# Kernel optimization log

Hardware: AMD Instinct MI355X
Metric: run time of the kernel (lower is better)

The kernel has to match this reference:

```python
import jax, jax.numpy as jnp
import numpy as np

T, B, C = 4, 2, 128
LT, LH, LW = 8, 32, 32
NUM_HEADS = 8
HEAD_DIM = C // NUM_HEADS
THETA = 0.7
V_TH = 1.0
TAU = 2.0  # spikingjelly LIFNode default tau
N_WIN = (2, 2, 2)
TOPK = 4
EPS = 1e-5
ATAN_ALPHA = 2.0  # spikingjelly surrogate.ATan default


@jax.custom_vjp
def spike(x):
    return (x >= 0.0).astype(x.dtype)

def _spike_fwd(x):
    return spike(x), x

def _spike_bwd(x, g):
    s = (jnp.pi / 2.0) * ATAN_ALPHA * x
    return (g * (ATAN_ALPHA / 2.0) / (1.0 + s * s),)

spike.defvjp(_spike_fwd, _spike_bwd)


def lif(x_seq):
    """Multi-step LIF: v'=v+(x-v)/tau, spike at v>=V_TH, hard reset to 0 (detached)."""
    def step(v, x):
        v = v + (x - v) / TAU
        s = spike(v - V_TH)
        v = v * (1.0 - jax.lax.stop_gradient(s))  # detach_reset, v_reset=0
        return v, s
    _, s_seq = jax.lax.scan(step, jnp.zeros_like(x_seq[0]), x_seq)
    return s_seq


def bn(x, gamma, beta):
    # BatchNorm3d(track_running_stats=False) on [T*B, C, D, H, W]: batch stats per channel
    mean = x.mean(axis=(0, 1, 3, 4, 5), keepdims=True)
    var = x.var(axis=(0, 1, 3, 4, 5), keepdims=True)
    shp = (1, 1, -1, 1, 1, 1)
    return (x - mean) * jax.lax.rsqrt(var + EPS) * gamma.reshape(shp) + beta.reshape(shp)


def conv3d(x, w, pad):
    t, b = x.shape[:2]
    y = jax.lax.conv_general_dilated(
        x.reshape((t * b,) + x.shape[2:]), w,
        window_strides=(1, 1, 1), padding=[(pad, pad)] * 3,
        dimension_numbers=('NCDHW', 'OIDHW', 'NCDHW'))
    return y.reshape((t, b) + y.shape[1:])


def cdc_t(x, w):
    out = conv3d(x, w, 1)
    # central-difference temporal term: 1x1x1 conv with summed first/last temporal slices
    kd = w[:, :, 0].sum((-1, -2)) + w[:, :, 2].sum((-1, -2))  # [O, I]
    return out - THETA * jnp.einsum('oi,tbidhw->tbodhw', kd, x)


def to_wins(t):
    wt, wh, ww = N_WIN
    Tn, Bn, Cn, Lt, Lh, Lw = t.shape
    lt, lh, lw = Lt // wt, Lh // wh, Lw // ww
    t = t.reshape(Tn, Bn, Cn, wt, lt, wh, lh, ww, lw)
    t = t.transpose(0, 1, 3, 5, 7, 4, 6, 8, 2)
    return t.reshape(Tn, Bn, wt * wh * ww, lt * lh * lw, Cn)


def setup_inputs() -> dict:
    key = jax.random.key(0)
    ks = jax.random.split(key, 4)
    x = jax.random.normal(ks[0], (T, B, C, LT, LH, LW), jnp.float32)
    qw = jax.random.normal(ks[1], (C, C, 3, 3, 3), jnp.float32) / np.sqrt(C * 27)
    kw = jax.random.normal(ks[2], (C, C), jnp.float32) / np.sqrt(C)
    pw = jax.random.normal(ks[3], (C, C), jnp.float32) / np.sqrt(C)
    ones = jnp.ones((C,), jnp.float32)
    zeros = jnp.zeros((C,), jnp.float32)
    return {"x": x, "qw": qw, "q_gamma": ones, "q_beta": zeros,
            "kw": kw, "k_gamma": ones, "k_beta": zeros,
            "v_gamma": ones, "v_beta": zeros,
            "pw": pw, "p_gamma": ones, "p_beta": zeros}


def reference(x, qw, q_gamma, q_beta, kw, k_gamma, k_beta,
              v_gamma, v_beta, pw, p_gamma, p_beta):
    Tn, Bn, Cn, Lt, Lh, Lw = x.shape
    wt, wh, ww = N_WIN
    num_wins = wt * wh * ww
    lt, lh, lw = Lt // wt, Lh // wh, Lw // ww

    q_real = bn(cdc_t(x, qw), q_gamma, q_beta)
    k_real = bn(jnp.einsum('oi,tbidhw->tbodhw', kw, x), k_gamma, k_beta)

    # region-level routing from pre-spike activations
    q_region = to_wins(q_real).mean(axis=(0, 3))  # [B, W, C]
    k_region = to_wins(k_real).mean(axis=(0, 3))
    a_r = jnp.einsum('bwc,bvc->bwv', q_region, k_region) * (HEAD_DIM ** -0.5)
    k_eff = min(TOPK, num_wins)
    _, idx = jax.lax.top_k(a_r, k_eff)  # [B, W, k]

    q = lif(q_real)
    k = lif(k_real)
    v = lif(bn(x, v_gamma, v_beta))
    q_w = to_wins(q)  # [T,B,W,S,C]
    k_w = to_wins(k)
    v_w = to_wins(v)

    # gather routed windows per (batch, target window), mean-aggregate over top-k
    gather = jax.vmap(lambda src_b, idx_b: src_b[:, idx_b], in_axes=(1, 0), out_axes=1)
    k_agg = gather(k_w, idx).mean(axis=3)  # [T,B,W,S,C]
    v_agg = gather(v_w, idx).mean(axis=3)

    S = q_w.shape[3]
    q_h = q_w.reshape(Tn, Bn, num_wins, S, NUM_HEADS, HEAD_DIM)
    k_h = k_agg.reshape(Tn, Bn, num_wins, S, NUM_HEADS, HEAD_DIM)
    v_h = v_agg.reshape(Tn, Bn, num_wins, S, NUM_HEADS, HEAD_DIM)

    attn = (q_h * k_h).sum(axis=5, keepdims=True)  # [T,B,W,S,H,1]
    attn = lif(attn)
    out = (attn * v_h).reshape(Tn, Bn, num_wins, S, Cn)

    out = out.reshape(Tn, Bn, wt, wh, ww, lt, lh, lw, Cn)
    out = out.transpose(0, 1, 8, 2, 5, 3, 6, 4, 7).reshape(Tn, Bn, Cn, Lt, Lh, Lw)

    out = lif(out)
    out = bn(jnp.einsum('oi,tbidhw->tbodhw', pw, out), p_gamma, p_beta)
    return out
```

## Files before the change

kernel.cpp:

```cpp
#include <hip/hip_runtime.h>

#define TT 4
#define BB 2
#define CC 128
#define DD 8
#define HHH 32
#define WWW 32
#define PP (DD*HHH*WWW)
#define TSTRIDE (BB*CC*PP)
#define NWIN 8
#define SSS 1024
#define NHEAD 8
#define HDIM 16
#define THETA 0.7f
#define VTH 1.0f
#define NPERC (TT*BB*PP)
#define EPSf 1e-5f

typedef unsigned short ushortT;
typedef _Float16 half_t;
typedef _Float16 f16x8 __attribute__((ext_vector_type(8)));
typedef float    f32x16 __attribute__((ext_vector_type(16)));

typedef const __attribute__((address_space(1))) void* as1_cvp;
typedef __attribute__((address_space(3))) void* as3_vp;

__global__ __launch_bounds__(256) void prep_wmodT(const float* __restrict__ qw,
                                                  float* __restrict__ wmodT) {
    int oi = blockIdx.x*256 + threadIdx.x;
    if (oi >= CC*CC) return;
    int o  = oi >> 7;
    int ic = oi & 127;
    const float* wp = qw + (size_t)oi*27;
    float kd = 0.f;
    #pragma unroll
    for (int t=0; t<9; t++) kd += wp[t] + wp[18+t];
    #pragma unroll
    for (int t=0; t<27; t++) {
        float v = wp[t] - ((t==13) ? THETA*kd : 0.f);
        wmodT[((size_t)o*27 + t)*CC + ic] = v;
    }
}

__global__ __launch_bounds__(256) void prep_wfrag(const float* __restrict__ wmodT,
                                                  half_t* __restrict__ wfrag) {
    int id = blockIdx.x*256 + threadIdx.x;
    if (id >= 8*27*4*64) return;
    int lane = id & 63;
    int r = id >> 6;
    int m = r & 3; r >>= 2;
    int t = r % 27;
    int kb = r / 27;
    int o   = m*32 + (lane & 31);
    int ic0 = kb*16 + (lane>>5)*8;
    size_t base = ((size_t)(id>>6))*2*64*8 + (size_t)lane*8;
    #pragma unroll
    for (int j=0;j<8;j++){
        float v = wmodT[((size_t)o*27 + t)*CC + ic0 + j];
        half_t h = (half_t)v;
        half_t l = (half_t)(v - (float)h);
        wfrag[base + 0*64*8 + j] = h;
        wfrag[base + 1*64*8 + j] = l;
    }
}

__global__ __launch_bounds__(256) void prep_w1frag(const float* __restrict__ W,
                                                   half_t* __restrict__ frag) {
    int id = blockIdx.x*256 + threadIdx.x;
    if (id >= 2048) return;
    int lane = id & 63;
    int r = id >> 6;
    int m = r & 3;
    int kb = r >> 2;
    int o   = m*32 + (lane & 31);
    int ic0 = kb*16 + (lane>>5)*8;
    size_t base = ((size_t)(kb*4+m))*2*64*8 + (size_t)lane*8;
    #pragma unroll
    for (int j=0;j<8;j++){
        float v = W[(size_t)o*CC + ic0 + j];
        half_t h = (half_t)v;
        half_t l = (half_t)(v - (float)h);
        frag[base + 0*64*8 + j] = h;
        frag[base + 1*64*8 + j] = l;
    }
}

__global__ __launch_bounds__(256) void build_xsplit(const float* __restrict__ x,
                                                    half_t* __restrict__ xsp) {
    int id = blockIdx.x*256 + threadIdx.x;
    if (id >= 8*16*8*34*34) return;
    int wt = id % 34; int r = id/34;
    int hp = r % 34;  r /= 34;
    int dz = r % 8;   r /= 8;
    int icg = r & 15; int tb = r >> 4;
    bool inb = (hp>=1) & (hp<=32) & (wt>=1) & (wt<=32);
    half_t h8[8], l8[8];
    #pragma unroll
    for (int j=0;j<8;j++){
        float v = 0.f;
        if (inb)
            v = x[((size_t)(tb*CC + icg*8+j))*PP + (size_t)dz*1024 + (hp-1)*32 + (wt-1)];
        half_t h = (half_t)v;
        half_t l = (half_t)(v - (float)h);
        h8[j]=h; l8[j]=l;
    }
    #pragma unroll
    for (int sp=0; sp<2; sp++){
        size_t gu = (((((size_t)tb*2 + sp)*16 + icg)*8 + dz)*34 + hp)*34 + wt;
        half_t* dst = xsp + gu*8;
        const half_t* src = (sp==0)?h8:l8;
        #pragma unroll
        for (int j=0;j<8;j++) dst[j] = src[j];
    }
}

__global__ __launch_bounds__(256,2) void conv_mfma2(const half_t* __restrict__ xsp,
                                                    const half_t* __restrict__ wfrag,
                                                    float* __restrict__ y0,
                                                    float* __restrict__ y1) {
    __shared__ half_t slab[3264*8];
    int tid  = threadIdx.x;
    int wid  = tid >> 6;
    int lane = tid & 63;
    int ln   = lane & 31;
    int half_ = lane >> 5;
    int hg = blockIdx.x;
    int dp = blockIdx.y;
    int z  = blockIdx.z;
    int tb = z >> 1, kh = z & 1;
    int H0 = hg*4, d0 = dp*2;
    float* y = kh ? y1 : y0;

    f32x16 acc[2][4];
    #pragma unroll
    for (int dt=0;dt<2;dt++)
        #pragma unroll
        for (int m=0;m<4;m++)
            #pragma unroll
            for (int i=0;i<16;i++) acc[dt][m][i] = 0.f;

    f16x8 ca[4][2];
    #pragma unroll
    for (int m=0;m<4;m++)
        #pragma unroll
        for (int sp=0;sp<2;sp++)
            ca[m][sp] = *(const f16x8*)&wfrag[((((size_t)(kh*4*27)*4 + m)*2+sp)*64 + lane)*8];

    #pragma unroll 1
    for (int kk=0; kk<4; kk++) {
        int kb = kh*4 + kk;
        __syncthreads();
        #pragma unroll 1
        for (int u = tid; u < 3264; u += 256) {
            int sp  = u / 1632;
            int r   = u - sp*1632;
            int icg = r / 816;
            int p   = r - icg*816;
            int dz  = p / 204;
            int r3  = p - dz*204;
            int hp  = r3 / 34;
            int wt  = r3 - hp*34;
            int dd  = d0 - 1 + dz;
            half_t* ldst = &slab[(size_t)u*8];
            if ((unsigned)dd < 8u) {
                size_t gu = (((((size_t)tb*2 + sp)*16 + (kb*2+icg))*8 + dd)*34 + (H0+hp))*34 + wt;
                __builtin_amdgcn_global_load_lds((as1_cvp)&xsp[gu*8], (as3_vp)ldst, 16, 0, 0);
            } else {
                ulonglong2 zz; zz.x = 0; zz.y = 0;
                *(ulonglong2*)ldst = zz;
            }
        }
        __syncthreads();
        #pragma unroll 1
        for (int t=0; t<27; t++) {
            int dz=t/9; int rr=t-dz*9; int dh=rr/3; int dw=rr-dh*3;
            f16x8 cb[2][2];
            #pragma unroll
            for (int dt=0;dt<2;dt++){
                int bpos = (dt+dz)*204 + (wid+dh)*34 + ln + dw;
                #pragma unroll
                for (int sp=0;sp<2;sp++)
                    cb[dt][sp] = *(const f16x8*)&slab[(size_t)((sp*2+half_)*816 + bpos)*8];
            }
            f16x8 na[4][2];
            int nt  = (t<26)? t+1 : 0;
            int nkb = (t<26)? kb  : ((kk<3)? kb+1 : kb);
            #pragma unroll
            for (int m=0;m<4;m++)
                #pragma unroll
                for (int sp=0;sp<2;sp++)
                    na[m][sp] = *(const f16x8*)&wfrag[((((size_t)(nkb*27+nt)*4+m)*2+sp)*64 + lane)*8];
            #pragma unroll
            for (int dt=0;dt<2;dt++)
                #pragma unroll
                for (int m=0;m<4;m++) acc[dt][m] = __builtin_amdgcn_mfma_f32_32x32x16_f16(ca[m][0], cb[dt][0], acc[dt][m],0,0,0);
            #pragma unroll
            for (int dt=0;dt<2;dt++)
                #pragma unroll
                for (int m=0;m<4;m++) acc[dt][m] = __builtin_amdgcn_mfma_f32_32x32x16_f16(ca[m][0], cb[dt][1], acc[dt][m],0,0,0);
            #pragma unroll
            for (int dt=0;dt<2;dt++)
                #pragma unroll
                for (int m=0;m<4;m++) acc[dt][m] = __builtin_amdgcn_mfma_f32_32x32x16_f16(ca[m][1], cb[dt][0], acc[dt][m],0,0,0);
            #pragma unroll
            for (int m=0;m<4;m++)
                #pragma unroll
                for (int sp=0;sp<2;sp++) ca[m][sp] = na[m][sp];
        }
    }
    int h = H0 + wid;
    #pragma unroll
    for (int dt=0; dt<2; dt++) {
        #pragma unroll
        for (int m=0; m<4; m++) {
            #pragma unroll
            for (int reg=0; reg<16; reg++) {
                int row = (reg&3) + 8*(reg>>2) + 4*half_;
                int o = m*32 + row;
                y[((size_t)tb*CC + o)*PP + (d0+dt)*1024 + h*32 + ln] = acc[dt][m][reg];
            }
        }
    }
}

__global__ __launch_bounds__(256) void conv_add(float* __restrict__ q,
                                                const float* __restrict__ p1) {
    size_t i = ((size_t)blockIdx.x*256 + threadIdx.x)*4;
    float4 a = *(const float4*)&q[i];
    float4 b = *(const float4*)&p1[i];
    a.x+=b.x; a.y+=b.y; a.z+=b.z; a.w+=b.w;
    *(float4*)&q[i] = a;
}

__global__ __launch_bounds__(256) void kgemm_mfma(const half_t* __restrict__ xsp,
                                                  const half_t* __restrict__ wk,
                                                  float* __restrict__ y) {
    int tid  = threadIdx.x;
    int wid  = tid >> 6;
    int lane = tid & 63;
    int ln   = lane & 31;
    int half_ = lane >> 5;
    int hg = blockIdx.x, d = blockIdx.y, tb = blockIdx.z;
    int h = hg*4 + wid;

    f32x16 acc[4];
    #pragma unroll
    for (int m=0;m<4;m++)
        #pragma unroll
        for (int i=0;i<16;i++) acc[m][i] = 0.f;

    #pragma unroll 2
    for (int kb=0; kb<8; kb++) {
        f16x8 b[2];
        #pragma unroll
        for (int sp=0; sp<2; sp++) {
            size_t gu = (((((size_t)tb*2 + sp)*16 + (kb*2+half_))*8 + d)*34 + (h+1))*34 + (ln+1);
            b[sp] = *(const f16x8*)&xsp[gu*8];
        }
        #pragma unroll
        for (int m=0; m<4; m++) {
            const half_t* wb = wk + ((size_t)(kb*4+m))*2*64*8 + (size_t)lane*8;
            f16x8 a0 = *(const f16x8*)&wb[0*64*8];
            f16x8 a1 = *(const f16x8*)&wb[1*64*8];
            acc[m] = __builtin_amdgcn_mfma_f32_32x32x16_f16(a0, b[0], acc[m],0,0,0);
            acc[m] = __builtin_amdgcn_mfma_f32_32x32x16_f16(a0, b[1], acc[m],0,0,0);
            acc[m] = __builtin_amdgcn_mfma_f32_32x32x16_f16(a1, b[0], acc[m],0,0,0);
        }
    }
    #pragma unroll
    for (int m=0; m<4; m++) {
        #pragma unroll
        for (int reg=0; reg<16; reg++) {
            int row = (reg&3) + 8*(reg>>2) + 4*half_;
            int o = m*32 + row;
            y[((size_t)tb*CC + o)*PP + d*1024 + h*32 + ln] = acc[m][reg];
        }
    }
}

__global__ __launch_bounds__(256) void pgemm_mfma(const ushortT* __restrict__ spkb,
                                                  const half_t* __restrict__ wp,
                                                  float* __restrict__ y) {
    int tid  = threadIdx.x;
    int wid  = tid >> 6;
    int lane = tid & 63;
    int ln   = lane & 31;
    int half_ = lane >> 5;
    int hg = blockIdx.x, d = blockIdx.y, tb = blockIdx.z;
    int h = hg*4 + wid;
    int p = d*1024 + h*32 + ln;

    f32x16 acc[4];
    #pragma unroll
    for (int m=0;m<4;m++)
        #pragma unroll
        for (int i=0;i<16;i++) acc[m][i] = 0.f;

    #pragma unroll 2
    for (int kb=0; kb<8; kb++) {
        f16x8 b = *(const f16x8*)&spkb[(((size_t)tb*16 + (kb*2+half_))*PP + p)*8];
        #pragma unroll
        for (int m=0; m<4; m++) {
            const half_t* wb = wp + ((size_t)(kb*4+m))*2*64*8 + (size_t)lane*8;
            f16x8 a0 = *(const f16x8*)&wb[0*64*8];
            f16x8 a1 = *(const f16x8*)&wb[1*64*8];
            acc[m] = __builtin_amdgcn_mfma_f32_32x32x16_f16(a0, b, acc[m],0,0,0);
            acc[m] = __builtin_amdgcn_mfma_f32_32x32x16_f16(a1, b, acc[m],0,0,0);
        }
    }
    #pragma unroll
    for (int m=0; m<4; m++) {
        #pragma unroll
        for (int reg=0; reg<16; reg++) {
            int row = (reg&3) + 8*(reg>>2) + 4*half_;
            int o = m*32 + row;
            y[((size_t)tb*CC + o)*PP + p] = acc[m][reg];
        }
    }
}

__global__ __launch_bounds__(128) void win_stats(const float* __restrict__ q,
        const float* __restrict__ k, const float* __restrict__ x,
        float* __restrict__ rsum, float* __restrict__ rsq) {
    int blk = blockIdx.x;
    int src = blk >> 11;
    int r   = blk & 2047;
    const float* base = (src==0) ? q : ((src==1) ? k : x);
    int c  = r & 127;
    int wi = (r >> 7) & 7;
    int b  = r >> 10;
    int wd = wi>>2, wh = (wi>>1)&1, ww = wi&1;
    int tid = threadIdx.x;
    float s=0.f, s2=0.f;
    for (int t=0;t<TT;t++){
        const float* p = base + ((size_t)(t*BB+b)*CC + c)*PP;
        for (int si=tid; si<SSS; si+=128){
            int ld = si>>8, lh=(si>>4)&15, lw=si&15;
            float v = p[((wd*4+ld)<<10) + ((wh*16+lh)<<5) + (ww*16+lw)];
            s += v; s2 += v*v;
        }
    }
    __shared__ float ls[128], ls2[128];
    ls[tid]=s; ls2[tid]=s2; __syncthreads();
    for (int off=64;off>0;off>>=1){
        if(tid<off){ ls[tid]+=ls[tid+off]; ls2[tid]+=ls2[tid+off]; }
        __syncthreads();
    }
    if (tid==0){ rsum[blk]=ls[0]; rsq[blk]=ls2[0]; }
}

__global__ __launch_bounds__(384) void stats_fin(const float* __restrict__ rsum,
        const float* __restrict__ rsq, float* __restrict__ sums) {
    int tid = threadIdx.x;
    int src = tid >> 7, c = tid & 127;
    float s=0.f, s2=0.f;
    for (int bw=0; bw<16; bw++){
        int idx = src*2048 + bw*128 + c;
        s  += rsum[idx];
        s2 += rsq[idx];
    }
    sums[src*256 + c]       = s;
    sums[src*256 + 128 + c] = s2;
}

__global__ __launch_bounds__(128) void route_topk(const float* __restrict__ qreg,
        const float* __restrict__ kreg,
        const float* __restrict__ qsum, const float* __restrict__ qsq,
        const float* __restrict__ ksum, const float* __restrict__ ksq,
        const float* __restrict__ qg, const float* __restrict__ qb,
        const float* __restrict__ kg, const float* __restrict__ kb,
        int* __restrict__ idxout) {
    __shared__ float qn[16*128], kn[16*128], ar[16*8];
    int tid = threadIdx.x;
    for (int e=tid; e<16*128; e+=128){
        int c = e&127;
        float qm = qsum[c]*(1.f/NPERC);
        float qv = qsq[c]*(1.f/NPERC) - qm*qm;
        float qr = rsqrtf(qv + EPSf);
        qn[e] = (qreg[e]*(1.f/(TT*SSS)) - qm)*qr*qg[c] + qb[c];
        float km = ksum[c]*(1.f/NPERC);
        float kv = ksq[c]*(1.f/NPERC) - km*km;
        float kr = rsqrtf(kv + EPSf);
        kn[e] = (kreg[e]*(1.f/(TT*SSS)) - km)*kr*kg[c] + kb[c];
    }
    __syncthreads();
    {
        int b = tid>>6, w=(tid>>3)&7, v=tid&7;
        float s=0.f;
        for (int c=0;c<128;c++) s += qn[(b*8+w)*128+c]*kn[(b*8+v)*128+c];
        ar[(b*8+w)*8+v] = s * 0.25f;
    }
    __syncthreads();
    if (tid < 16){
        const float* row = &ar[tid*8];
        bool used[8] = {false,false,false,false,false,false,false,false};
        for (int j=0;j<4;j++){
            int best=0; float bv=-3.0e38f;
            for (int v=0; v<8; v++){
                if (!used[v] && row[v] > bv){ bv=row[v]; best=v; }
            }
            used[best]=true;
            idxout[tid*4+j]=best;
        }
    }
}

__global__ __launch_bounds__(256) void lif_bn_win3(const float* __restrict__ qin,
        const float* __restrict__ kin, const float* __restrict__ xin,
        float* __restrict__ qs, float* __restrict__ ks, float* __restrict__ vs,
        const float* __restrict__ stats,
        const float* __restrict__ qg, const float* __restrict__ qb,
        const float* __restrict__ kg, const float* __restrict__ kb,
        const float* __restrict__ vg, const float* __restrict__ vb) {
    int src = blockIdx.y;
    const float* in  = (src==0) ? qin : ((src==1) ? kin : xin);
    float*       spk = (src==0) ? qs  : ((src==1) ? ks  : vs);
    const float* gamma = (src==0) ? qg : ((src==1) ? kg : vg);
    const float* beta  = (src==0) ? qb : ((src==1) ? kb : vb);
    int e = blockIdx.x*256 + threadIdx.x;
    if (e >= BB*CC*PP) return;
    int p = e & (PP-1);
    int c = (e >> 13) & 127;
    int b = e >> 20;
    float mean = stats[src*256 + c]*(1.f/NPERC);
    float var  = stats[src*256 + 128 + c]*(1.f/NPERC) - mean*mean;
    float sc = rsqrtf(var+EPSf)*gamma[c];
    float sh = beta[c] - mean*sc;
    int d = p>>10, h=(p>>5)&31, w=p&31;
    int wi = ((d>>2)*2 + (h>>4))*2 + (w>>4);
    int si = (((d&3)<<4) + (h&15))*16 + (w&15);
    size_t widx = ((size_t)(b*NWIN+wi)*CC + c)*SSS + si;
    float v=0.f;
    #pragma unroll
    for (int t=0;t<TT;t++){
        float xn = in[(size_t)t*TSTRIDE + e]*sc + sh;
        v = (v+xn)*0.5f;
        float s = (v>=VTH)?1.f:0.f;
        spk[(size_t)t*TSTRIDE + widx] = s;
        v *= (1.f - s);
    }
}

__global__ __launch_bounds__(256) void attn_lif(const float* __restrict__ qspk,
        const float* __restrict__ kspk, const float* __restrict__ vspk,
        const int* __restrict__ idx, ushortT* __restrict__ spkb) {
    int id = blockIdx.x*256 + threadIdx.x;
    if (id >= BB*NWIN*NHEAD*SSS) return;
    int s  = id & 1023;
    int hh = (id>>10) & 7;
    int wi = (id>>13) & 7;
    int b  = id>>16;
    int bw = b*NWIN+wi;
    size_t qbase = ((size_t)bw*CC + hh*HDIM)*SSS + s;
    size_t sbase[4];
    #pragma unroll
    for (int j=0;j<4;j++){
        int src = idx[bw*4+j];
        sbase[j] = ((size_t)(b*NWIN+src)*CC + hh*HDIM)*SSS + s;
    }
    int wd = wi>>2, wh = (wi>>1)&1, ww = wi&1;
    int d3 = wd*4 + (s>>8), h3 = wh*16 + ((s>>4)&15), w3 = ww*16 + (s&15);
    int p  = (d3<<10) + (h3<<5) + w3;

    float v=0.f;
    float v2[16];
    #pragma unroll
    for (int dd=0; dd<16; dd++) v2[dd]=0.f;

    #pragma unroll 1
    for (int t=0;t<TT;t++){
        size_t toff = (size_t)t*TSTRIDE;
        float km[16], vm[16];
        #pragma unroll
        for (int dd=0;dd<16;dd++){ km[dd]=0.f; vm[dd]=0.f; }
        #pragma unroll
        for (int j=0;j<4;j++){
            const float* kp = kspk+toff+sbase[j];
            const float* vp = vspk+toff+sbase[j];
            #pragma unroll
            for (int dd=0; dd<16; dd++){
                km[dd] += kp[(size_t)dd*SSS];
                vm[dd] += vp[(size_t)dd*SSS];
            }
        }
        const float* qp = qspk+toff+qbase;
        float att=0.f;
        #pragma unroll
        for (int dd=0;dd<16;dd++) att += qp[(size_t)dd*SSS]*km[dd];
        att *= 0.25f;
        v = (v+att)*0.5f;
        float sp = (v>=VTH)?1.f:0.f;
        v *= (1.f-sp);
        float spq = sp*0.25f;
        union { ushortT u[8]; uint4 q4; } pk0, pk1;
        #pragma unroll
        for (int dd=0;dd<16;dd++){
            float ov = spq*vm[dd];
            v2[dd] = (v2[dd]+ov)*0.5f;
            float s2 = (v2[dd]>=VTH)?1.f:0.f;
            v2[dd] *= (1.f-s2);
            ushortT bs = (s2 != 0.f) ? (ushortT)0x3C00 : (ushortT)0;
            if (dd < 8) pk0.u[dd] = bs; else pk1.u[dd-8] = bs;
        }
        int tb2 = t*BB + b;
        size_t base = (((size_t)tb2*16 + hh*2)*PP + p)*8;
        *(uint4*)&spkb[base] = pk0.q4;
        *(uint4*)&spkb[base + (size_t)PP*8] = pk1.q4;
    }
}

__global__ __launch_bounds__(256) void pstats_part(const float* __restrict__ xin,
        float* __restrict__ part_sum, float* __restrict__ part_sq) {
    int blk = blockIdx.x;
    int c = blk & 127, tb = blk >> 7;
    int tid = threadIdx.x;
    const float* p = xin + ((size_t)tb*CC + c)*PP;
    float s=0.f, s2=0.f;
    for (int i=tid; i<PP; i+=256){ float v=p[i]; s+=v; s2+=v*v; }
    __shared__ float ls[256], ls2[256];
    ls[tid]=s; ls2[tid]=s2; __syncthreads();
    for (int off=128; off>0; off>>=1){
        if (tid<off){ ls[tid]+=ls[tid+off]; ls2[tid]+=ls2[tid+off]; }
        __syncthreads();
    }
    if (tid==0){ part_sum[blk]=ls[0]; part_sq[blk]=ls2[0]; }
}

__global__ __launch_bounds__(128) void pstats_fin(const float* __restrict__ part_sum,
        const float* __restrict__ part_sq, float* __restrict__ sum,
        float* __restrict__ sq) {
    int c = threadIdx.x;
    float s=0.f, s2=0.f;
    for (int tb=0; tb<8; tb++){
        s  += part_sum[tb*128+c];
        s2 += part_sq[tb*128+c];
    }
    sum[c]=s; sq[c]=s2;
}

__global__ __launch_bounds__(256) void bn_apply(const float* __restrict__ xin,
        float* __restrict__ yout,
        const float* __restrict__ sum, const float* __restrict__ sq,
        const float* __restrict__ gamma, const float* __restrict__ beta) {
    size_t i = (size_t)blockIdx.x*256 + threadIdx.x;
    if (i >= (size_t)TT*BB*CC*PP) return;
    int c = (int)((i>>13)&127);
    float mean = sum[c]*(1.f/NPERC);
    float var  = sq[c]*(1.f/NPERC) - mean*mean;
    float sc = rsqrtf(var+EPSf)*gamma[c];
    float sh = beta[c] - mean*sc;
    yout[i] = xin[i]*sc + sh;
}

extern "C" void kernel_launch(void* const* d_in, const int* in_sizes, int n_in,
                              void* d_out, int out_size, void* d_ws, size_t ws_size,
                              hipStream_t stream) {
    const float* x  = (const float*)d_in[0];
    const float* qw = (const float*)d_in[1];
    const float* qg = (const float*)d_in[2];
    const float* qb = (const float*)d_in[3];
    const float* kw = (const float*)d_in[4];
    const float* kg = (const float*)d_in[5];
    const float* kb = (const float*)d_in[6];
    const float* vg = (const float*)d_in[7];
    const float* vb = (const float*)d_in[8];
    const float* pw = (const float*)d_in[9];
    const float* pg = (const float*)d_in[10];
    const float* pb = (const float*)d_in[11];
    float* out = (float*)d_out;
    float* ws  = (float*)d_ws;

    const size_t NEL = (size_t)TT*TSTRIDE;
    float* qconv = ws;
    float* kconv = ws + NEL;
    float* qspk  = ws + 2*NEL;
    float* kspk  = ws + 3*NEL;
    float* vspk  = ws + 4*NEL;
    float* wmodT = ws + 5*NEL;
    float* stats = ws + 5*NEL + 442368;
    float *qsum=stats,     *qsq=stats+128,  *ksum=stats+256, *ksq=stats+384,
          *psum=stats+768, *psq=stats+896;
    float* rsum = stats + 1024;
    float* rsq  = rsum + 6144;
    float* ppart_sum = rsq + 6144;
    float* ppart_sq  = ppart_sum + 1024;
    int*   idxp = (int*)(ppart_sq + 1024);

    half_t* xsp    = (half_t*)(ws + 2*NEL);
    half_t* wfrag  = (half_t*)(ws + 4*NEL);
    half_t* wkfrag = (half_t*)(ws + 4*NEL) + 884736;
    half_t* wpfrag = (half_t*)(ws + 4*NEL);
    ushortT* spkb  = (ushortT*)(ws + NEL);
    float*   pconv = ws + 2*NEL;
    float*   part1 = kconv;

    prep_wmodT<<<64,256,0,stream>>>(qw, wmodT);
    prep_wfrag<<<216,256,0,stream>>>(wmodT, wfrag);
    prep_w1frag<<<8,256,0,stream>>>(kw, wkfrag);
    build_xsplit<<<4624,256,0,stream>>>(x, xsp);
    {
        dim3 cg(8,4,16);
        conv_mfma2<<<cg,256,0,stream>>>(xsp, wfrag, qconv, part1);
    }
    conv_add<<<8192,256,0,stream>>>(qconv, part1);
    {
        dim3 gg(8,8,8);
        kgemm_mfma<<<gg,256,0,stream>>>(xsp, wkfrag, kconv);
    }
    win_stats<<<6144,128,0,stream>>>(qconv, kconv, x, rsum, rsq);
    stats_fin<<<1,384,0,stream>>>(rsum, rsq, stats);
    route_topk<<<1,128,0,stream>>>(rsum, rsum+2048, qsum,qsq,ksum,ksq,qg,qb,kg,kb,idxp);
    {
        dim3 lg(8192,3);
        lif_bn_win3<<<lg,256,0,stream>>>(qconv,kconv,x, qspk,kspk,vspk,
                                         stats, qg,qb,kg,kb,vg,vb);
    }
    attn_lif<<<512,256,0,stream>>>(qspk,kspk,vspk,idxp,spkb);
    prep_w1frag<<<8,256,0,stream>>>(pw, wpfrag);
    {
        dim3 gg(8,8,8);
        pgemm_mfma<<<gg,256,0,stream>>>(spkb, wpfrag, pconv);
    }
    pstats_part<<<1024,256,0,stream>>>(pconv, ppart_sum, ppart_sq);
    pstats_fin<<<1,128,0,stream>>>(ppart_sum, ppart_sq, psum, psq);
    bn_apply<<<32768,256,0,stream>>>(pconv, out, psum, psq, pg, pb);
}
```

Before: 408.9 us.

## Double-buffer conv input slabs in LDS with async loads and larger depth tiles

The 3x3x3 MFMA convolution kernel now uses 512-thread blocks that each cover four depth slices instead of two. This halves the relative depth-halo reloads per block. Input slabs are staged into a double-buffered dynamic-LDS region with global_load_lds, and explicit vmcnt waits plus s_barrier let the next channel block's load overlap the MFMA loop on the current one. Out-of-range depth rows now load from a zero halo row of the split buffer instead of being written as explicit zeros. The roughly 156KB LDS footprint allows only one block per CU and a grid of only 256 blocks, which may limit latency hiding.

```diff
diff --git a/kernel.cpp b/kernel.cpp
--- a/kernel.cpp
+++ b/kernel.cpp
@@ -114,11 +114,11 @@
     }
 }
 
-__global__ __launch_bounds__(256,2) void conv_mfma2(const half_t* __restrict__ xsp,
+__global__ __launch_bounds__(512,2) void conv_mfma3(const half_t* __restrict__ xsp,
                                                     const half_t* __restrict__ wfrag,
                                                     float* __restrict__ y0,
                                                     float* __restrict__ y1) {
-    __shared__ half_t slab[3264*8];
+    extern __shared__ half_t slab[];
     int tid  = threadIdx.x;
     int wid  = tid >> 6;
     int lane = tid & 63;
@@ -128,8 +128,33 @@
     int dp = blockIdx.y;
     int z  = blockIdx.z;
     int tb = z >> 1, kh = z & 1;
-    int H0 = hg*4, d0 = dp*2;
+    int H0 = hg*4, d0 = dp*4;
+    int r  = wid & 3;
+    int q  = wid >> 2;
     float* y = kh ? y1 : y0;
+
+    auto STAGE = [&](int bk, int bsel) {
+        int kb = kh*4 + bk;
+        half_t* bufp = slab + (size_t)bsel*(4896*8);
+        #pragma unroll 1
+        for (int k2=0; k2<10; k2++) {
+            int u = tid + (k2<<9);
+            if (u < 4896) {
+                int sp  = (u >= 2448) ? 1 : 0;
+                int r1  = u - sp*2448;
+                int icg = (r1 >= 1224) ? 1 : 0;
+                int p2  = r1 - icg*1224;
+                int dzs = p2/204; int r3 = p2 - dzs*204;
+                int hp  = r3/34;  int wt = r3 - hp*34;
+                int dd  = d0 - 1 + dzs;
+                const half_t* src = ((unsigned)dd < 8u)
+                    ? &xsp[((((((size_t)tb*2 + sp)*16 + (kb*2+icg))*8 + dd)*34 + (H0+hp))*34 + wt)*8]
+                    : &xsp[(size_t)ln*8];
+                __builtin_amdgcn_global_load_lds((as1_cvp)src,
+                    (as3_vp)(bufp + (size_t)u*8), 16, 0, 0);
+            }
+        }
+    };
 
     f32x16 acc[2][4];
     #pragma unroll
@@ -145,42 +170,34 @@
         #pragma unroll
         for (int sp=0;sp<2;sp++)
             ca[m][sp] = *(const f16x8*)&wfrag[((((size_t)(kh*4*27)*4 + m)*2+sp)*64 + lane)*8];
+
+    asm volatile("" ::: "memory");
+    STAGE(0,0);
+    STAGE(1,1);
+    asm volatile("" ::: "memory");
 
     #pragma unroll 1
     for (int kk=0; kk<4; kk++) {
         int kb = kh*4 + kk;
-        __syncthreads();
-        #pragma unroll 1
-        for (int u = tid; u < 3264; u += 256) {
-            int sp  = u / 1632;
-            int r   = u - sp*1632;
-            int icg = r / 816;
-            int p   = r - icg*816;
-            int dz  = p / 204;
-            int r3  = p - dz*204;
-            int hp  = r3 / 34;
-            int wt  = r3 - hp*34;
-            int dd  = d0 - 1 + dz;
-            half_t* ldst = &slab[(size_t)u*8];
-            if ((unsigned)dd < 8u) {
-                size_t gu = (((((size_t)tb*2 + sp)*16 + (kb*2+icg))*8 + dd)*34 + (H0+hp))*34 + wt;
-                __builtin_amdgcn_global_load_lds((as1_cvp)&xsp[gu*8], (as3_vp)ldst, 16, 0, 0);
-            } else {
-                ulonglong2 zz; zz.x = 0; zz.y = 0;
-                *(ulonglong2*)ldst = zz;
-            }
-        }
-        __syncthreads();
+        if (kk == 0) {
+            if (wid < 5) asm volatile("s_waitcnt vmcnt(10)" ::: "memory");
+            else         asm volatile("s_waitcnt vmcnt(9)"  ::: "memory");
+        } else {
+            asm volatile("s_waitcnt vmcnt(63)" ::: "memory");
+        }
+        __builtin_amdgcn_s_barrier();
+        asm volatile("" ::: "memory");
+        const half_t* bufp = slab + (size_t)(kk&1)*(4896*8);
         #pragma unroll 1
         for (int t=0; t<27; t++) {
             int dz=t/9; int rr=t-dz*9; int dh=rr/3; int dw=rr-dh*3;
             f16x8 cb[2][2];
             #pragma unroll
             for (int dt=0;dt<2;dt++){
-                int bpos = (dt+dz)*204 + (wid+dh)*34 + ln + dw;
+                int unitb = (q*2 + dt + dz)*204 + (r+dh)*34 + (ln+dw);
                 #pragma unroll
                 for (int sp=0;sp<2;sp++)
-                    cb[dt][sp] = *(const f16x8*)&slab[(size_t)((sp*2+half_)*816 + bpos)*8];
+                    cb[dt][sp] = *(const f16x8*)&bufp[(size_t)((sp*2+half_)*1224 + unitb)*8];
             }
             f16x8 na[4][2];
             int nt  = (t<26)? t+1 : 0;
@@ -207,17 +224,23 @@
                 #pragma unroll
                 for (int sp=0;sp<2;sp++) ca[m][sp] = na[m][sp];
         }
-    }
-    int h = H0 + wid;
+        asm volatile("" ::: "memory");
+        __builtin_amdgcn_s_barrier();
+        asm volatile("" ::: "memory");
+        if (kk < 2) STAGE(kk+2, kk&1);
+    }
+
+    int h = H0 + r;
     #pragma unroll
     for (int dt=0; dt<2; dt++) {
+        int d = d0 + q*2 + dt;
         #pragma unroll
         for (int m=0; m<4; m++) {
             #pragma unroll
             for (int reg=0; reg<16; reg++) {
                 int row = (reg&3) + 8*(reg>>2) + 4*half_;
                 int o = m*32 + row;
-                y[((size_t)tb*CC + o)*PP + (d0+dt)*1024 + h*32 + ln] = acc[dt][m][reg];
+                y[((size_t)tb*CC + o)*PP + d*1024 + h*32 + ln] = acc[dt][m][reg];
             }
         }
     }
@@ -599,8 +622,15 @@
     prep_w1frag<<<8,256,0,stream>>>(kw, wkfrag);
     build_xsplit<<<4624,256,0,stream>>>(x, xsp);
     {
-        dim3 cg(8,4,16);
-        conv_mfma2<<<cg,256,0,stream>>>(xsp, wfrag, qconv, part1);
+        static bool attr_set = false;
+        const int shmem = 2*4896*8*(int)sizeof(half_t);
+        if (!attr_set) {
+            hipFuncSetAttribute((const void*)conv_mfma3,
+                                hipFuncAttributeMaxDynamicSharedMemorySize, shmem);
+            attr_set = true;
+        }
+        dim3 cg(8,2,16);
+        conv_mfma3<<<cg,512,shmem,stream>>>(xsp, wfrag, qconv, part1);
     }
     conv_add<<<8192,256,0,stream>>>(qconv, part1);
     {
```

Result: no change. 407.9 us (-0.3%).
